# Kernel tuning notes

Hardware: AMD Instinct MI355X
Metric: run time of the kernel (lower is better)

Reference implementation:

```python
import jax, jax.numpy as jnp
import numpy as np

B, H, S, D = 4, 16, 2048, 64
ROPE_BASE = 10000.0


def _rope(x):
    # Rotate-half RoPE over the last dim, positions along the second-to-last dim.
    d = x.shape[-1]
    s = x.shape[-2]
    inv_freq = 1.0 / (ROPE_BASE ** (jnp.arange(0, d, 2, dtype=jnp.float32) / d))  # [D/2]
    ang = jnp.arange(s, dtype=jnp.float32)[:, None] * inv_freq                    # [S, D/2]
    cos, sin = jnp.cos(ang), jnp.sin(ang)
    x1, x2 = x[..., : d // 2], x[..., d // 2:]
    return jnp.concatenate([x1 * cos - x2 * sin, x1 * sin + x2 * cos], axis=-1).astype(x.dtype)


def setup_inputs() -> dict:
    key = jax.random.key(0)
    kq, kk, kv = jax.random.split(key, 3)
    q = jax.random.normal(kq, (B, H, S, D), dtype=jnp.float32)
    k = jax.random.normal(kk, (B, H, S, D), dtype=jnp.float32)
    v = jax.random.normal(kv, (B, H, S, D), dtype=jnp.float32)
    mask = jnp.tril(jnp.ones((S, S), dtype=bool))  # causal, broadcasts over [B,H,S,S]
    return {"q": q, "k": k, "v": v, "mask": mask}


def reference(q, k, v, mask):
    d_k = q.shape[-1]
    qr = _rope(q)
    kr = _rope(k)
    scores = jnp.einsum('bhqd,bhkd->bhqk', qr, kr) / jnp.sqrt(jnp.asarray(d_k, jnp.float32))
    scores = jnp.where(mask, scores, -jnp.inf)  # masked_fill(mask == False, -inf)
    probs = jax.nn.softmax(scores, axis=-1)
    return jnp.einsum('bhqk,bhkd->bhqd', probs, v)
```

## Files before the change

kernel.cpp:

```cpp
#include <hip/hip_runtime.h>
#include <hip/hip_bf16.h>
#include <math.h>

#define SS 2048
#define DD 64
#define BH 64
#define KT 64
#define NT 256
#define NKT (SS / KT)
#define QTT 128
#define NTA 256
#define NPAIR 8
#define LQ 72
#define LOG2E 1.4426950408889634f
#define IFS (13.287712379549449f / 32.0f)

typedef __attribute__((ext_vector_type(8))) short s8v;
typedef __attribute__((ext_vector_type(4))) short s4v;
typedef __attribute__((ext_vector_type(4))) float f4v;

__device__ __forceinline__ short f2b(float x) {
  __hip_bfloat16 h = __float2bfloat16(x);
  return *reinterpret_cast<short*>(&h);
}

__device__ __forceinline__ void gload16(const void* g, void* l) {
  __builtin_amdgcn_global_load_lds(
      (const __attribute__((address_space(1))) void*)g,
      (__attribute__((address_space(3))) void*)l, 16, 0, 0);
}

template <int CTRL>
__device__ __forceinline__ float dppf(float x) {
  int i = __builtin_bit_cast(int, x);
  i = __builtin_amdgcn_update_dpp(i, i, CTRL, 0xf, 0xf, false);
  return __builtin_bit_cast(float, i);
}
__device__ __forceinline__ float rowmax16(float x) {
  x = fmaxf(x, dppf<0xB1>(x));
  x = fmaxf(x, dppf<0x4E>(x));
  x = fmaxf(x, dppf<0x124>(x));
  x = fmaxf(x, dppf<0x128>(x));
  return x;
}
__device__ __forceinline__ float rowsum16(float x) {
  x += dppf<0xB1>(x);
  x += dppf<0x4E>(x);
  x += dppf<0x124>(x);
  x += dppf<0x128>(x);
  return x;
}

__device__ __forceinline__ void rope_cs(int pos, int j, float& c, float& s) {
  float inv = exp2f(-(float)j * IFS);
  float ang = (float)pos * inv;
  __sincosf(ang, &s, &c);
}

__global__ __launch_bounds__(NT) void prep_kv_kernel(
    const float* __restrict__ kg, const float* __restrict__ vg,
    short* __restrict__ kr, short* __restrict__ vt) {
  __shared__ float Vs[KT][DD + 1];
  const int b = blockIdx.x;
  const int kt = b & 31;
  const int t = threadIdx.x;
  const size_t ofs = (size_t)b * (KT * DD);
  const float* ktile = kg + ofs;
  short* krt = kr + ofs;

#pragma unroll
  for (int i = 0; i < 8; ++i) {
    int idx = t + i * NT;
    int r = idx >> 5, j = idx & 31;
    float s, c;
    rope_cs(kt * KT + r, j, c, s);
    float x1 = ktile[r * DD + j], x2 = ktile[r * DD + j + 32];
    krt[r * DD + j] = f2b(x1 * c - x2 * s);
    krt[r * DD + j + 32] = f2b(x1 * s + x2 * c);
  }

  const float* vtile = vg + ofs;
#pragma unroll
  for (int i = 0; i < 4; ++i) {
    int s4 = t + i * NT;
    int r = s4 >> 4, c4 = (s4 & 15) * 4;
    float4 v = *(const float4*)&vtile[r * DD + c4];
    Vs[r][c4 + 0] = v.x;
    Vs[r][c4 + 1] = v.y;
    Vs[r][c4 + 2] = v.z;
    Vs[r][c4 + 3] = v.w;
  }
  __syncthreads();
  short* otile = vt + ofs;
#pragma unroll
  for (int i = 0; i < 2; ++i) {
    int c = t + i * NT;
    int d = c >> 3, k8 = (c & 7) * 8;
    s8v o;
#pragma unroll
    for (int u = 0; u < 8; ++u) {
      int kp = k8 + u;
      int src = ((kp & 31) >> 3) * 4 + (kp & 3) +
                ((kp >> 5) * 2 + ((kp >> 2) & 1)) * 16;
      o[u] = f2b(Vs[src][d]);
    }
    *(s8v*)&otile[d * KT + k8] = o;
  }
}

__global__ __launch_bounds__(NTA, 2) void attn_fast(
    const float* __restrict__ qg, const short* __restrict__ kr,
    const short* __restrict__ vt, float* __restrict__ og) {
  __shared__ __align__(16) short Ks[2][KT * DD];
  __shared__ __align__(16) short Vts[2][DD * KT];
  __shared__ __align__(16) short QQ[2][QTT * DD];

  const int tid = threadIdx.x;
  const int lane = tid & 63;
  const int wv = tid >> 6;
  const int quad = lane >> 4;
  const int lx = lane & 15;
  const int xb = lx & 7;
  const int foff0 = ((quad ^ xb) << 3);
  const int foff1 = (((quad | 4) ^ xb) << 3);

  const int bid = blockIdx.x;
  const int g = bid >> 6;
  const int bh = bid & 63;
  const int qbA = 15 - g;
  const int qbB = g;
  const float* Q = qg + (size_t)bh * SS * DD;
  float* O = og + (size_t)bh * SS * DD;
  const short* krh = kr + (size_t)bh * SS * DD;
  const short* vth = vt + (size_t)bh * SS * DD;

  int goff[2], loff[2];
#pragma unroll
  for (int i = 0; i < 2; ++i) {
    int c = wv * 128 + i * 64 + lane;
    int r = c >> 3, qp = c & 7;
    int qs = qp ^ (r & 7);
    goff[i] = r * DD + qs * 8;
    loff[i] = (wv * 128 + i * 64) * 8;
  }

#pragma unroll
  for (int i = 0; i < 2; ++i) {
    gload16(krh + goff[i], &Ks[0][loff[i]]);
    gload16(vth + goff[i], &Vts[0][loff[i]]);
  }

  const float qscale = 0.125f * LOG2E;
  for (int t = 0; t < 32; ++t) {
    int idx = tid + t * NTA;
    int r = idx >> 5, j = idx & 31;
    int ph = r >> 7, rr = r & 127;
    int grow = (ph ? qbB : qbA) * QTT + rr;
    float s, c;
    rope_cs(grow, j, c, s);
    float x1 = Q[(size_t)grow * DD + j];
    float x2 = Q[(size_t)grow * DD + j + 32];
    short* dst = &QQ[ph][0];
    int rb = rr & 7;
    dst[rr * DD + ((((j >> 3) ^ rb) << 3) | (j & 7))] = f2b((x1 * c - x2 * s) * qscale);
    dst[rr * DD + (((((j >> 3) | 4) ^ rb) << 3) | (j & 7))] = f2b((x1 * s + x2 * c) * qscale);
  }
  __syncthreads();

  s8v qx0[2], qx1[2];
#pragma unroll
  for (int h = 0; h < 2; ++h) {
    const int rq = wv * 32 + h * 16 + lx;
    qx0[h] = *(const s8v*)&QQ[0][rq * DD + foff0];
    qx1[h] = *(const s8v*)&QQ[0][rq * DD + foff1];
  }

  const short bone = f2b(1.0f);
  s8v ones;
#pragma unroll
  for (int u = 0; u < 8; ++u) ones[u] = bone;

  f4v o_[2][4];
  f4v ol[2];
#pragma unroll
  for (int h = 0; h < 2; ++h) {
    ol[h] = (f4v){0.f, 0.f, 0.f, 0.f};
#pragma unroll
    for (int db = 0; db < 4; ++db) o_[h][db] = (f4v){0.f, 0.f, 0.f, 0.f};
  }

  int qb = qbA;
  int ktend = 2 * qbA + 1;
  int mykt = 2 * qbA + (wv >> 1);
  int kt = 0;
  const int NIT = 34;

  for (int it = 0; it < NIT; ++it) {
    const int cur = it & 1;
    __syncthreads();

    if (it < NIT - 1) {
      const int nt = (kt < ktend) ? kt + 1 : 0;
      const short* ktile = krh + (size_t)nt * (KT * DD);
      const short* vtile = vth + (size_t)nt * (DD * KT);
#pragma unroll
      for (int i = 0; i < 2; ++i) {
        gload16(ktile + goff[i], &Ks[cur ^ 1][loff[i]]);
        gload16(vtile + goff[i], &Vts[cur ^ 1][loff[i]]);
      }
    }

    if (kt <= mykt) {
      f4v sc[2][4];
#pragma unroll
      for (int nb = 0; nb < 4; ++nb) {
        const int rk = nb * 16 + lx;
        s8v kf0 = *(const s8v*)&Ks[cur][rk * DD + foff0];
        s8v kf1 = *(const s8v*)&Ks[cur][rk * DD + foff1];
#pragma unroll
        for (int h = 0; h < 2; ++h) {
          f4v z = (f4v){0.f, 0.f, 0.f, 0.f};
          z = __builtin_amdgcn_mfma_f32_16x16x32_bf16(kf0, qx0[h], z, 0, 0, 0);
          z = __builtin_amdgcn_mfma_f32_16x16x32_bf16(kf1, qx1[h], z, 0, 0, 0);
          sc[h][nb] = z;
        }
      }

      if (kt == mykt) {
#pragma unroll
        for (int h = 0; h < 2; ++h) {
          const int thr = (wv & 1) * 32 + h * 16 + lx;
#pragma unroll
          for (int nb = 0; nb < 4; ++nb)
#pragma unroll
            for (int r = 0; r < 4; ++r)
              if (nb * 16 + quad * 4 + r > thr) sc[h][nb][r] = -INFINITY;
        }
      }

      s8v pf0[2], pf1[2];
#pragma unroll
      for (int h = 0; h < 2; ++h) {
#pragma unroll
        for (int nb = 0; nb < 4; ++nb)
#pragma unroll
          for (int r = 0; r < 4; ++r) {
            short pb = f2b(__builtin_amdgcn_exp2f(sc[h][nb][r]));
            if (nb < 2) pf0[h][nb * 4 + r] = pb;
            else        pf1[h][(nb - 2) * 4 + r] = pb;
          }
        ol[h] = __builtin_amdgcn_mfma_f32_16x16x32_bf16(pf0[h], ones, ol[h], 0, 0, 0);
        ol[h] = __builtin_amdgcn_mfma_f32_16x16x32_bf16(pf1[h], ones, ol[h], 0, 0, 0);
      }

#pragma unroll
      for (int db = 0; db < 4; ++db) {
        const int rv = db * 16 + lx;
        s8v vf0 = *(const s8v*)&Vts[cur][rv * KT + foff0];
        s8v vf1 = *(const s8v*)&Vts[cur][rv * KT + foff1];
#pragma unroll
        for (int h = 0; h < 2; ++h) {
          o_[h][db] = __builtin_amdgcn_mfma_f32_16x16x32_bf16(pf0[h], vf0, o_[h][db], 0, 0, 0);
          o_[h][db] = __builtin_amdgcn_mfma_f32_16x16x32_bf16(pf1[h], vf1, o_[h][db], 0, 0, 0);
        }
      }
    }

    ++kt;
    if (kt > ktend && it < NIT - 1) {
#pragma unroll
      for (int h = 0; h < 2; ++h)
#pragma unroll
        for (int r = 0; r < 4; ++r) {
          float rinv = 1.0f / ol[h][r];
          int row = qb * QTT + wv * 32 + h * 16 + quad * 4 + r;
#pragma unroll
          for (int db = 0; db < 4; ++db)
            O[(size_t)row * DD + db * 16 + lx] = o_[h][db][r] * rinv;
        }
#pragma unroll
      for (int h = 0; h < 2; ++h) {
        ol[h] = (f4v){0.f, 0.f, 0.f, 0.f};
#pragma unroll
        for (int db = 0; db < 4; ++db) o_[h][db] = (f4v){0.f, 0.f, 0.f, 0.f};
        const int rq = wv * 32 + h * 16 + lx;
        qx0[h] = *(const s8v*)&QQ[1][rq * DD + foff0];
        qx1[h] = *(const s8v*)&QQ[1][rq * DD + foff1];
      }
      qb = qbB;
      ktend = 2 * qbB + 1;
      mykt = 2 * qbB + (wv >> 1);
      kt = 0;
    }
  }

#pragma unroll
  for (int h = 0; h < 2; ++h)
#pragma unroll
    for (int r = 0; r < 4; ++r) {
      float rinv = 1.0f / ol[h][r];
      int row = qb * QTT + wv * 32 + h * 16 + quad * 4 + r;
#pragma unroll
      for (int db = 0; db < 4; ++db)
        O[(size_t)row * DD + db * 16 + lx] = o_[h][db][r] * rinv;
    }
}

__global__ __launch_bounds__(NT, 4) void attn_fallback(
    const float* __restrict__ qg, const float* __restrict__ kg,
    const float* __restrict__ vg, float* __restrict__ og) {
  __shared__ __align__(16) short Qs[64 * LQ];
  __shared__ __align__(16) short Ksh[64 * LQ];
  __shared__ __align__(16) short Vt[DD * LQ];
  __shared__ __align__(16) short Ps[4][16 * LQ];

  const int tid = threadIdx.x;
  const int lane = tid & 63;
  const int wv = tid >> 6;
  const int quad = lane >> 4;
  const int lx = lane & 15;

  const int bid = blockIdx.x;
  const int qt = NKT - 1 - (bid >> 6);
  const int bh = bid & 63;
  const int qbase = qt * 64;
  const size_t base = (size_t)bh * SS * DD;
  const float* Q = qg + base;
  const float* K = kg + base;
  const float* V = vg + base;
  float* O = og + base;

  const float qscale = 0.125f * LOG2E;
  for (int t = 0; t < 8; ++t) {
    int idx = tid + t * NT;
    int r = idx >> 5, j = idx & 31;
    float c, s;
    rope_cs(qbase + r, j, c, s);
    float x1 = Q[(size_t)(qbase + r) * DD + j];
    float x2 = Q[(size_t)(qbase + r) * DD + j + 32];
    Qs[r * LQ + j] = f2b((x1 * c - x2 * s) * qscale);
    Qs[r * LQ + j + 32] = f2b((x1 * s + x2 * c) * qscale);
  }
  __syncthreads();

  s8v qf0 = *(const s8v*)&Qs[(wv * 16 + lx) * LQ + quad * 8];
  s8v qf1 = *(const s8v*)&Qs[(wv * 16 + lx) * LQ + 32 + quad * 8];

  float m_[4], l_[4];
  f4v o_[4];
#pragma unroll
  for (int r = 0; r < 4; ++r) { m_[r] = -INFINITY; l_[r] = 0.f; }
#pragma unroll
  for (int db = 0; db < 4; ++db) o_[db] = (f4v){0.f, 0.f, 0.f, 0.f};

  for (int kt = 0; kt <= qt; ++kt) {
    const int kbase = kt * 64;
    __syncthreads();
    for (int t = 0; t < 8; ++t) {
      int idx = tid + t * NT;
      int r = idx >> 5, j = idx & 31;
      float c, s;
      rope_cs(kbase + r, j, c, s);
      float x1 = K[(size_t)(kbase + r) * DD + j];
      float x2 = K[(size_t)(kbase + r) * DD + j + 32];
      Ksh[r * LQ + j] = f2b(x1 * c - x2 * s);
      Ksh[r * LQ + j + 32] = f2b(x1 * s + x2 * c);
    }
    for (int t = 0; t < 4; ++t) {
      int i4 = tid + t * NT;
      int r = i4 >> 4, c4 = (i4 & 15) * 4;
      const float4 v = *(const float4*)&V[(size_t)(kbase + r) * DD + c4];
      Vt[(c4 + 0) * LQ + r] = f2b(v.x);
      Vt[(c4 + 1) * LQ + r] = f2b(v.y);
      Vt[(c4 + 2) * LQ + r] = f2b(v.z);
      Vt[(c4 + 3) * LQ + r] = f2b(v.w);
    }
    __syncthreads();

    f4v sc[4];
#pragma unroll
    for (int nb = 0; nb < 4; ++nb) {
      s8v kf0 = *(const s8v*)&Ksh[(nb * 16 + lx) * LQ + quad * 8];
      s8v kf1 = *(const s8v*)&Ksh[(nb * 16 + lx) * LQ + 32 + quad * 8];
      f4v z = (f4v){0.f, 0.f, 0.f, 0.f};
      z = __builtin_amdgcn_mfma_f32_16x16x32_bf16(qf0, kf0, z, 0, 0, 0);
      z = __builtin_amdgcn_mfma_f32_16x16x32_bf16(qf1, kf1, z, 0, 0, 0);
      sc[nb] = z;
    }
    if (kt == qt) {
#pragma unroll
      for (int nb = 0; nb < 4; ++nb)
#pragma unroll
        for (int r = 0; r < 4; ++r)
          if (kbase + nb * 16 + lx > qbase + wv * 16 + quad * 4 + r)
            sc[nb][r] = -INFINITY;
    }
#pragma unroll
    for (int r = 0; r < 4; ++r) {
      float mx = fmaxf(fmaxf(sc[0][r], sc[1][r]), fmaxf(sc[2][r], sc[3][r]));
      mx = rowmax16(mx);
      float mn = fmaxf(m_[r], mx);
      float al = __builtin_amdgcn_exp2f(m_[r] - mn);
      m_[r] = mn;
      float rs = 0.f;
#pragma unroll
      for (int nb = 0; nb < 4; ++nb) {
        float p = __builtin_amdgcn_exp2f(sc[nb][r] - mn);
        rs += p;
        Ps[wv][(quad * 4 + r) * LQ + nb * 16 + lx] = f2b(p);
      }
      rs = rowsum16(rs);
      l_[r] = l_[r] * al + rs;
      o_[0][r] *= al; o_[1][r] *= al; o_[2][r] *= al; o_[3][r] *= al;
    }
    s8v pf0 = *(const s8v*)&Ps[wv][lx * LQ + quad * 8];
    s8v pf1 = *(const s8v*)&Ps[wv][lx * LQ + 32 + quad * 8];
#pragma unroll
    for (int db = 0; db < 4; ++db) {
      s8v vf0 = *(const s8v*)&Vt[(db * 16 + lx) * LQ + quad * 8];
      s8v vf1 = *(const s8v*)&Vt[(db * 16 + lx) * LQ + 32 + quad * 8];
      o_[db] = __builtin_amdgcn_mfma_f32_16x16x32_bf16(pf0, vf0, o_[db], 0, 0, 0);
      o_[db] = __builtin_amdgcn_mfma_f32_16x16x32_bf16(pf1, vf1, o_[db], 0, 0, 0);
    }
  }
#pragma unroll
  for (int r = 0; r < 4; ++r) {
    float rinv = 1.0f / l_[r];
    int row = qbase + wv * 16 + quad * 4 + r;
#pragma unroll
    for (int db = 0; db < 4; ++db)
      O[(size_t)row * DD + db * 16 + lx] = o_[db][r] * rinv;
  }
}

extern "C" void kernel_launch(void* const* d_in, const int* in_sizes, int n_in,
                              void* d_out, int out_size, void* d_ws, size_t ws_size,
                              hipStream_t stream) {
  const float* q = (const float*)d_in[0];
  const float* k = (const float*)d_in[1];
  const float* v = (const float*)d_in[2];
  float* out = (float*)d_out;

  const size_t kr_bytes = (size_t)BH * SS * DD * sizeof(short);
  const size_t vt_bytes = kr_bytes;
  const size_t need = kr_bytes + vt_bytes;

  if (ws_size >= need) {
    short* kr = (short*)d_ws;
    short* vt = (short*)((char*)d_ws + kr_bytes);
    prep_kv_kernel<<<BH * NKT, NT, 0, stream>>>(k, v, kr, vt);
    attn_fast<<<dim3(BH * NPAIR), dim3(NTA), 0, stream>>>(q, kr, vt, out);
  } else {
    attn_fallback<<<dim3(BH * NKT), dim3(NT), 0, stream>>>(q, k, v, out);
  }
}
```

Before: 186.6 us.

## Triple-buffer K/V tiles with prefetch distance two and explicit vmcnt waits

Expands the K/V shared-memory ring from two to three buffers and issues global-to-LDS loads two iterations ahead. A partial s_waitcnt vmcnt(4) before the barrier replaces the full drain, so one tile's loads can stay in flight while the current tile is computed. It also raises wave priority around the MFMA section with s_setprio. The extra LDS buffer may reduce occupancy under the 2-blocks-per-CU launch bound, and the hand-written vmcnt count must match the number of outstanding loads.

```diff
diff --git a/kernel.cpp b/kernel.cpp
--- a/kernel.cpp
+++ b/kernel.cpp
@@ -111,8 +111,8 @@
 __global__ __launch_bounds__(NTA, 2) void attn_fast(
     const float* __restrict__ qg, const short* __restrict__ kr,
     const short* __restrict__ vt, float* __restrict__ og) {
-  __shared__ __align__(16) short Ks[2][KT * DD];
-  __shared__ __align__(16) short Vts[2][DD * KT];
+  __shared__ __align__(16) short Ks[3][KT * DD];
+  __shared__ __align__(16) short Vts[3][DD * KT];
   __shared__ __align__(16) short QQ[2][QTT * DD];
 
   const int tid = threadIdx.x;
@@ -129,6 +129,8 @@
   const int bh = bid & 63;
   const int qbA = 15 - g;
   const int qbB = g;
+  const int nitA = 2 * qbA + 2;
+  const int NIT = 34;
   const float* Q = qg + (size_t)bh * SS * DD;
   float* O = og + (size_t)bh * SS * DD;
   const short* krh = kr + (size_t)bh * SS * DD;
@@ -148,6 +150,15 @@
   for (int i = 0; i < 2; ++i) {
     gload16(krh + goff[i], &Ks[0][loff[i]]);
     gload16(vth + goff[i], &Vts[0][loff[i]]);
+  }
+  {
+    const short* ktile = krh + (size_t)1 * (KT * DD);
+    const short* vtile = vth + (size_t)1 * (DD * KT);
+#pragma unroll
+    for (int i = 0; i < 2; ++i) {
+      gload16(ktile + goff[i], &Ks[1][loff[i]]);
+      gload16(vtile + goff[i], &Vts[1][loff[i]]);
+    }
   }
 
   const float qscale = 0.125f * LOG2E;
@@ -193,24 +204,35 @@
   int ktend = 2 * qbA + 1;
   int mykt = 2 * qbA + (wv >> 1);
   int kt = 0;
-  const int NIT = 34;
+  int cur = 0;
 
   for (int it = 0; it < NIT; ++it) {
-    const int cur = it & 1;
-    __syncthreads();
-
     if (it < NIT - 1) {
-      const int nt = (kt < ktend) ? kt + 1 : 0;
-      const short* ktile = krh + (size_t)nt * (KT * DD);
-      const short* vtile = vth + (size_t)nt * (DD * KT);
-#pragma unroll
-      for (int i = 0; i < 2; ++i) {
-        gload16(ktile + goff[i], &Ks[cur ^ 1][loff[i]]);
-        gload16(vtile + goff[i], &Vts[cur ^ 1][loff[i]]);
+      asm volatile("s_waitcnt vmcnt(4)" ::: "memory");
+    } else {
+      asm volatile("s_waitcnt vmcnt(0)" ::: "memory");
+    }
+    __builtin_amdgcn_sched_barrier(0);
+    __builtin_amdgcn_s_barrier();
+    __builtin_amdgcn_sched_barrier(0);
+
+    {
+      int p = it + 2;
+      if (p < NIT) {
+        int tp = (p < nitA) ? p : p - nitA;
+        int nb3 = cur + 2; if (nb3 >= 3) nb3 -= 3;
+        const short* ktile = krh + (size_t)tp * (KT * DD);
+        const short* vtile = vth + (size_t)tp * (DD * KT);
+#pragma unroll
+        for (int i = 0; i < 2; ++i) {
+          gload16(ktile + goff[i], &Ks[nb3][loff[i]]);
+          gload16(vtile + goff[i], &Vts[nb3][loff[i]]);
+        }
       }
     }
 
     if (kt <= mykt) {
+      __builtin_amdgcn_s_setprio(1);
       f4v sc[2][4];
 #pragma unroll
       for (int nb = 0; nb < 4; ++nb) {
@@ -264,8 +286,10 @@
           o_[h][db] = __builtin_amdgcn_mfma_f32_16x16x32_bf16(pf1[h], vf1, o_[h][db], 0, 0, 0);
         }
       }
-    }
-
+      __builtin_amdgcn_s_setprio(0);
+    }
+
+    ++cur; if (cur >= 3) cur -= 3;
     ++kt;
     if (kt > ktend && it < NIT - 1) {
 #pragma unroll
```

Result: no change. 187.6 us (+0.5%).
